# Kernel tuning notes

Measured on AMD Instinct MI355X. Metric: run time of the kernel, lower is better.

Reference implementation:

```python
import jax, jax.numpy as jnp
import numpy as np

D_MODEL = 512
FACTOR = 1
B, L = 32, 2048


def setup_inputs() -> dict:
    key = jax.random.key(0)
    kq, kk, kv = jax.random.split(key, 3)
    query = jax.random.normal(kq, (B, L, D_MODEL), dtype=jnp.float32)
    key_t = jax.random.normal(kk, (B, L, D_MODEL), dtype=jnp.float32)
    value = jax.random.normal(kv, (B, L, D_MODEL), dtype=jnp.float32)
    return {"query": query, "key": key_t, "value": value}


def reference(query, key, value):
    d = D_MODEL
    # FFT-based autocorrelation along the feature (last) axis
    q_fft = jnp.fft.rfft(query, n=d, axis=-1)
    k_fft = jnp.fft.rfft(key, n=d, axis=-1)
    corr = jnp.fft.irfft(q_fft * jnp.conj(k_fft), n=d, axis=-1)  # [B, L, d]

    # top_k = int(factor * log(L)); static because shapes are static
    top_k = int(FACTOR * np.log(value.shape[1]))
    top_vals, _ = jax.lax.top_k(corr, top_k)                      # [B, L, top_k]
    mean_value = jnp.mean(top_vals, axis=-1, keepdims=True)       # [B, L, 1]

    # softmax over the (corr, mean) pair per element
    stacked = jnp.stack(
        [corr, jnp.broadcast_to(mean_value, corr.shape)], axis=-1)  # [B, L, d, 2]
    weights = jax.nn.softmax(stacked, axis=-1)

    # roll values by -1 along the time axis (double-transpose roll in TF source)
    rolled = jnp.roll(value, shift=-1, axis=1)
    out = value * weights[..., 0] + rolled * weights[..., 1]
    return out
```

## Files before the change

kernel.cpp:

```cpp
#include <hip/hip_runtime.h>
#include <math.h>


#define LBITS 11
#define LMASK 2047

typedef float2 cplx;

__device__ __forceinline__ cplx cmul(cplx a, cplx b) {
  return make_float2(a.x * b.x - a.y * b.y, a.x * b.y + a.y * b.x);
}
__device__ __forceinline__ cplx cadd(cplx a, cplx b) {
  return make_float2(a.x + b.x, a.y + b.y);
}
__device__ __forceinline__ cplx csub(cplx a, cplx b) {
  return make_float2(a.x - b.x, a.y - b.y);
}
__device__ __forceinline__ cplx csel(bool c, cplx a, cplx b) {
  return make_float2(c ? a.x : b.x, c ? a.y : b.y);
}
__device__ __forceinline__ cplx cmuli(cplx a, float S) {
  return make_float2(-S * a.y, S * a.x);
}

__device__ __forceinline__ int bitrev6(int x) {
  return (int)(__brev((unsigned)x) >> 26);
}

template<int SIGN>
__device__ __forceinline__ void dft8(cplx* x) {
  const float R = 0.70710678118654752f;
  const float S = (float)SIGN;
  cplx t0 = cadd(x[0], x[4]), t4 = csub(x[0], x[4]);
  cplx t1 = cadd(x[1], x[5]), d1 = csub(x[1], x[5]);
  cplx t2 = cadd(x[2], x[6]), d2 = csub(x[2], x[6]);
  cplx t3 = cadd(x[3], x[7]), d3 = csub(x[3], x[7]);
  cplx t5 = cmul(d1, make_float2(R, S * R));
  cplx t6 = cmuli(d2, S);
  cplx t7 = cmul(d3, make_float2(-R, S * R));
  cplx u0 = cadd(t0, t2), u2 = csub(t0, t2);
  cplx u1 = cadd(t1, t3), u3 = cmuli(csub(t1, t3), S);
  cplx u4 = cadd(t4, t6), u6 = csub(t4, t6);
  cplx u5 = cadd(t5, t7), u7 = cmuli(csub(t5, t7), S);
  cplx v0 = cadd(u0, u1), v1 = csub(u0, u1);
  cplx v2 = cadd(u2, u3), v3 = csub(u2, u3);
  cplx v4 = cadd(u4, u5), v5 = csub(u4, u5);
  cplx v6 = cadd(u6, u7), v7 = csub(u6, u7);
  x[0] = v0; x[1] = v4; x[2] = v2; x[3] = v6;
  x[4] = v1; x[5] = v5; x[6] = v3; x[7] = v7;
}

__device__ __forceinline__ void lane_fft64_dif_fwd(cplx* v, int lane) {
#pragma unroll
  for (int s = 5; s >= 0; --s) {
    const int m = 1 << s;
    const bool hi = (lane & m) != 0;
    float sn, cs;
    __sincosf(-(float)M_PI / (float)m * (float)(lane & (m - 1)), &sn, &cs);
    const cplx w = make_float2(cs, sn);
#pragma unroll
    for (int j = 0; j < 8; ++j) {
      cplx x = v[j], p;
      p.x = __shfl_xor(x.x, m);
      p.y = __shfl_xor(x.y, m);
      cplx sum = cadd(x, p);
      cplx dif = csub(p, x);
      v[j] = csel(hi, cmul(dif, w), sum);
    }
  }
}

__device__ __forceinline__ void lane_fft64_dit_inv(cplx* v, int lane) {
#pragma unroll
  for (int s = 0; s <= 5; ++s) {
    const int m = 1 << s;
    const bool hi = (lane & m) != 0;
    float sn, cs;
    __sincosf((float)M_PI / (float)m * (float)(lane & (m - 1)), &sn, &cs);
    const cplx w = make_float2(cs, sn);
#pragma unroll
    for (int j = 0; j < 8; ++j) {
      cplx x = v[j], p;
      p.x = __shfl_xor(x.x, m);
      p.y = __shfl_xor(x.y, m);
      cplx even = csel(hi, p, x);
      cplx odd  = csel(hi, x, p);
      cplx t = cmul(odd, w);
      v[j] = csel(hi, csub(even, t), cadd(even, t));
    }
  }
}

extern "C" __global__ void __launch_bounds__(256)
autocorr_kernel(const float* __restrict__ q, const float* __restrict__ k,
                const float* __restrict__ vv, float* __restrict__ out) {
  const int lane = (int)threadIdx.x & 63;
  const int wid = (int)threadIdx.x >> 6;
  const int p = (int)blockIdx.x * 4 + wid;
  const int b = p >> LBITS;
  const int l = p & LMASK;
  const size_t base = (size_t)p * 512;

  cplx v[8];
#pragma unroll
  for (int j = 0; j < 8; ++j) {
    const int n = lane + 64 * j;
    v[j] = make_float2(q[base + n], k[base + n]);
  }

  dft8<-1>(v);
  {
    float sn, cs;
    __sincosf(-2.0f * (float)M_PI * (float)lane / 512.0f, &sn, &cs);
    const cplx bw = make_float2(cs, sn);
    cplx w = bw;
#pragma unroll
    for (int j = 1; j < 8; ++j) { v[j] = cmul(v[j], w); w = cmul(w, bw); }
  }
  lane_fft64_dif_fwd(v, lane);

  cplx Bc[8];
#pragma unroll
  for (int k2 = 1; k2 < 8; ++k2) {
    Bc[k2].x = __shfl_xor(v[8 - k2].x, 63);
    Bc[k2].y = __shfl_xor(v[8 - k2].y, 63);
  }
  {
    const int src = bitrev6((64 - bitrev6(lane)) & 63);
    Bc[0].x = __shfl(v[0].x, src);
    Bc[0].y = __shfl(v[0].y, src);
  }

  const float sc = 0.25f / 512.0f;
#pragma unroll
  for (int j = 0; j < 8; ++j) {
    const cplx A = v[j], B = Bc[j];
    const float sr = sc * ((A.x + B.x) * (A.y + B.y) - (A.y - B.y) * (A.x - B.x));
    const float si = sc * ((A.x * A.x - B.x * B.x) + (A.y * A.y - B.y * B.y));
    v[j] = make_float2(sr, si);
  }

  lane_fft64_dit_inv(v, lane);
  {
    float sn, cs;
    __sincosf(2.0f * (float)M_PI * (float)lane / 512.0f, &sn, &cs);
    const cplx bw = make_float2(cs, sn);
    cplx w = bw;
#pragma unroll
    for (int j = 1; j < 8; ++j) { v[j] = cmul(v[j], w); w = cmul(w, bw); }
  }
  dft8<1>(v);

  float vals[8];
#pragma unroll
  for (int j = 0; j < 8; ++j) vals[j] = v[j].x;

  const int pn = (b << LBITS) | ((l + 1) & LMASK);
  const size_t basen = (size_t)pn * 512;
  float va[8], vb[8];
#pragma unroll
  for (int j = 0; j < 8; ++j) {
    const int n = lane + 64 * j;
    va[j] = vv[base + n];
    vb[j] = vv[basen + n];
  }

  float tmp[8];
#pragma unroll
  for (int i = 0; i < 8; ++i) tmp[i] = vals[i];
  float ssum = 0.0f;
  for (int r = 0; r < 7; ++r) {
    float mloc = tmp[0];
#pragma unroll
    for (int i = 1; i < 8; ++i) mloc = fmaxf(mloc, tmp[i]);
    float g = mloc;
#pragma unroll
    for (int off = 32; off >= 1; off >>= 1) g = fmaxf(g, __shfl_xor(g, off));
    ssum += g;
    const unsigned long long ball = __ballot(mloc == g);
    const int firstlane = (int)__ffsll(ball) - 1;
    if (lane == firstlane) {
      bool done = false;
#pragma unroll
      for (int i = 0; i < 8; ++i) {
        if (!done && tmp[i] == g) { tmp[i] = -1e30f; done = true; }
      }
    }
  }
  const float mean = ssum * (1.0f / 7.0f);

#pragma unroll
  for (int j = 0; j < 8; ++j) {
    const float w1 = 1.0f / (1.0f + __expf(vals[j] - mean));
    out[base + lane + 64 * j] = va[j] + (vb[j] - va[j]) * w1;
  }
}

extern "C" void kernel_launch(void* const* d_in, const int* in_sizes, int n_in,
                              void* d_out, int out_size, void* d_ws, size_t ws_size,
                              hipStream_t stream) {
  const float* q = (const float*)d_in[0];
  const float* k = (const float*)d_in[1];
  const float* v = (const float*)d_in[2];
  float* out = (float*)d_out;
  const int positions = 32 * 2048;
  autocorr_kernel<<<dim3(positions / 4), dim3(256), 0, stream>>>(q, k, v, out);
}
```

Before: 444.1 us.

## Use DPP/swizzle cross-lane ops, precomputed twiddles, and threshold-based top-k

```diff
diff --git a/kernel.cpp b/kernel.cpp
--- a/kernel.cpp
+++ b/kernel.cpp
@@ -8,7 +8,7 @@
 typedef float2 cplx;
 
 __device__ __forceinline__ cplx cmul(cplx a, cplx b) {
-  return make_float2(a.x * b.x - a.y * b.y, a.x * b.y + a.y * b.x);
+  return make_float2(fmaf(a.x, b.x, -(a.y * b.y)), fmaf(a.x, b.y, a.y * b.x));
 }
 __device__ __forceinline__ cplx cadd(cplx a, cplx b) {
   return make_float2(a.x + b.x, a.y + b.y);
@@ -16,15 +16,31 @@
 __device__ __forceinline__ cplx csub(cplx a, cplx b) {
   return make_float2(a.x - b.x, a.y - b.y);
 }
-__device__ __forceinline__ cplx csel(bool c, cplx a, cplx b) {
-  return make_float2(c ? a.x : b.x, c ? a.y : b.y);
-}
 __device__ __forceinline__ cplx cmuli(cplx a, float S) {
   return make_float2(-S * a.y, S * a.x);
 }
 
 __device__ __forceinline__ int bitrev6(int x) {
   return (int)(__brev((unsigned)x) >> 26);
+}
+
+template<int M>
+__device__ __forceinline__ float shx(float x, int a32) {
+  const int xi = __float_as_int(x);
+  int r;
+  if constexpr (M == 1)
+    r = __builtin_amdgcn_update_dpp(xi, xi, 0xB1, 0xF, 0xF, false);
+  else if constexpr (M == 2)
+    r = __builtin_amdgcn_update_dpp(xi, xi, 0x4E, 0xF, 0xF, false);
+  else if constexpr (M == 4)
+    r = __builtin_amdgcn_ds_swizzle(xi, 0x101F);
+  else if constexpr (M == 8)
+    r = __builtin_amdgcn_ds_swizzle(xi, 0x201F);
+  else if constexpr (M == 16)
+    r = __builtin_amdgcn_ds_swizzle(xi, 0x401F);
+  else
+    r = __builtin_amdgcn_ds_bpermute(a32, xi);
+  return __int_as_float(r);
 }
 
 template<int SIGN>
@@ -50,45 +66,52 @@
   x[4] = v1; x[5] = v5; x[6] = v3; x[7] = v7;
 }
 
-__device__ __forceinline__ void lane_fft64_dif_fwd(cplx* v, int lane) {
-#pragma unroll
-  for (int s = 5; s >= 0; --s) {
-    const int m = 1 << s;
-    const bool hi = (lane & m) != 0;
-    float sn, cs;
-    __sincosf(-(float)M_PI / (float)m * (float)(lane & (m - 1)), &sn, &cs);
-    const cplx w = make_float2(cs, sn);
-#pragma unroll
-    for (int j = 0; j < 8; ++j) {
-      cplx x = v[j], p;
-      p.x = __shfl_xor(x.x, m);
-      p.y = __shfl_xor(x.y, m);
-      cplx sum = cadd(x, p);
-      cplx dif = csub(p, x);
-      v[j] = csel(hi, cmul(dif, w), sum);
+template<int M>
+__device__ __forceinline__ void fwd_stage(cplx* v, float2 weff, float sgn, int a32) {
+#pragma unroll
+  for (int j = 0; j < 8; ++j) {
+    const float px = shx<M>(v[j].x, a32);
+    const float py = shx<M>(v[j].y, a32);
+    const float prx = fmaf(v[j].x, sgn, px);
+    const float pry = fmaf(v[j].y, sgn, py);
+    if constexpr (M == 1) {
+      v[j] = make_float2(prx, pry);
+    } else {
+      v[j] = make_float2(fmaf(prx, weff.x, -(pry * weff.y)),
+                         fmaf(prx, weff.y, pry * weff.x));
     }
   }
 }
 
-__device__ __forceinline__ void lane_fft64_dit_inv(cplx* v, int lane) {
-#pragma unroll
-  for (int s = 0; s <= 5; ++s) {
-    const int m = 1 << s;
-    const bool hi = (lane & m) != 0;
-    float sn, cs;
-    __sincosf((float)M_PI / (float)m * (float)(lane & (m - 1)), &sn, &cs);
-    const cplx w = make_float2(cs, sn);
-#pragma unroll
-    for (int j = 0; j < 8; ++j) {
-      cplx x = v[j], p;
-      p.x = __shfl_xor(x.x, m);
-      p.y = __shfl_xor(x.y, m);
-      cplx even = csel(hi, p, x);
-      cplx odd  = csel(hi, x, p);
-      cplx t = cmul(odd, w);
-      v[j] = csel(hi, csub(even, t), cadd(even, t));
+template<int M>
+__device__ __forceinline__ void inv_stage(cplx* v, float2 weff, float sgn, int a32) {
+#pragma unroll
+  for (int j = 0; j < 8; ++j) {
+    float ux, uy;
+    if constexpr (M == 1) {
+      ux = v[j].x; uy = v[j].y;
+    } else {
+      ux = fmaf(v[j].x, weff.x, v[j].y * weff.y);
+      uy = fmaf(v[j].y, weff.x, -(v[j].x * weff.y));
     }
-  }
+    const float px = shx<M>(ux, a32);
+    const float py = shx<M>(uy, a32);
+    v[j] = make_float2(fmaf(ux, sgn, px), fmaf(uy, sgn, py));
+  }
+}
+
+__device__ __forceinline__ float wave_max63(float v) {
+#define DPP_MAX(ctrl)                                                        \
+  v = fmaxf(v, __int_as_float(__builtin_amdgcn_update_dpp(                   \
+                   __float_as_int(v), __float_as_int(v), ctrl, 0xF, 0xF, false)));
+  DPP_MAX(0x111)
+  DPP_MAX(0x112)
+  DPP_MAX(0x114)
+  DPP_MAX(0x118)
+  DPP_MAX(0x142)
+  DPP_MAX(0x143)
+#undef DPP_MAX
+  return __int_as_float(__builtin_amdgcn_readlane(__float_as_int(v), 63));
 }
 
 extern "C" __global__ void __launch_bounds__(256)
@@ -101,6 +124,26 @@
   const int l = p & LMASK;
   const size_t base = (size_t)p * 512;
 
+  const int a32 = ((lane ^ 32) << 2);
+  const int a63 = ((lane ^ 63) << 2);
+  const int a0h = (bitrev6((64 - bitrev6(lane)) & 63) << 2);
+
+  float2 w32, w16, w8, w4, w2;
+  {
+    float sn, cs;
+#define MKW(dst, m)                                                          \
+    __sincosf(-(float)M_PI * (float)(lane & ((m)-1)) / (float)(m), &sn, &cs);\
+    dst = (lane & (m)) ? make_float2(cs, sn) : make_float2(1.0f, 0.0f);
+    MKW(w32, 32) MKW(w16, 16) MKW(w8, 8) MKW(w4, 4) MKW(w2, 2)
+#undef MKW
+  }
+  const float s32 = (lane & 32) ? -1.0f : 1.0f;
+  const float s16 = (lane & 16) ? -1.0f : 1.0f;
+  const float s8  = (lane & 8)  ? -1.0f : 1.0f;
+  const float s4  = (lane & 4)  ? -1.0f : 1.0f;
+  const float s2  = (lane & 2)  ? -1.0f : 1.0f;
+  const float s1  = (lane & 1)  ? -1.0f : 1.0f;
+
   cplx v[8];
 #pragma unroll
   for (int j = 0; j < 8; ++j) {
@@ -109,45 +152,54 @@
   }
 
   dft8<-1>(v);
+  float2 bw;
   {
     float sn, cs;
     __sincosf(-2.0f * (float)M_PI * (float)lane / 512.0f, &sn, &cs);
-    const cplx bw = make_float2(cs, sn);
+    bw = make_float2(cs, sn);
     cplx w = bw;
 #pragma unroll
     for (int j = 1; j < 8; ++j) { v[j] = cmul(v[j], w); w = cmul(w, bw); }
   }
-  lane_fft64_dif_fwd(v, lane);
+  fwd_stage<32>(v, w32, s32, a32);
+  fwd_stage<16>(v, w16, s16, a32);
+  fwd_stage<8>(v, w8, s8, a32);
+  fwd_stage<4>(v, w4, s4, a32);
+  fwd_stage<2>(v, w2, s2, a32);
+  fwd_stage<1>(v, w2, s1, a32);
 
   cplx Bc[8];
 #pragma unroll
   for (int k2 = 1; k2 < 8; ++k2) {
-    Bc[k2].x = __shfl_xor(v[8 - k2].x, 63);
-    Bc[k2].y = __shfl_xor(v[8 - k2].y, 63);
-  }
+    Bc[k2].x = __int_as_float(__builtin_amdgcn_ds_bpermute(a63, __float_as_int(v[8 - k2].x)));
+    Bc[k2].y = __int_as_float(__builtin_amdgcn_ds_bpermute(a63, __float_as_int(v[8 - k2].y)));
+  }
+  Bc[0].x = __int_as_float(__builtin_amdgcn_ds_bpermute(a0h, __float_as_int(v[0].x)));
+  Bc[0].y = __int_as_float(__builtin_amdgcn_ds_bpermute(a0h, __float_as_int(v[0].y)));
+
+  const float sc = 0.25f / 512.0f;
+#pragma unroll
+  for (int j = 0; j < 8; ++j) {
+    const cplx A = v[j], B = Bc[j];
+    const float t1 = A.x + B.x, t2 = A.y + B.y, t3 = A.y - B.y, t4 = A.x - B.x;
+    const float sr = sc * fmaf(t1, t2, -(t3 * t4));
+    float si = fmaf(A.x, A.x, -(B.x * B.x));
+    si = fmaf(A.y, A.y, si);
+    si = fmaf(-B.y, B.y, si);
+    v[j] = make_float2(sr, sc * si);
+  }
+
+  inv_stage<1>(v, w2, s1, a32);
+  inv_stage<2>(v, w2, s2, a32);
+  inv_stage<4>(v, w4, s4, a32);
+  inv_stage<8>(v, w8, s8, a32);
+  inv_stage<16>(v, w16, s16, a32);
+  inv_stage<32>(v, w32, s32, a32);
   {
-    const int src = bitrev6((64 - bitrev6(lane)) & 63);
-    Bc[0].x = __shfl(v[0].x, src);
-    Bc[0].y = __shfl(v[0].y, src);
-  }
-
-  const float sc = 0.25f / 512.0f;
-#pragma unroll
-  for (int j = 0; j < 8; ++j) {
-    const cplx A = v[j], B = Bc[j];
-    const float sr = sc * ((A.x + B.x) * (A.y + B.y) - (A.y - B.y) * (A.x - B.x));
-    const float si = sc * ((A.x * A.x - B.x * B.x) + (A.y * A.y - B.y * B.y));
-    v[j] = make_float2(sr, si);
-  }
-
-  lane_fft64_dit_inv(v, lane);
-  {
-    float sn, cs;
-    __sincosf(2.0f * (float)M_PI * (float)lane / 512.0f, &sn, &cs);
-    const cplx bw = make_float2(cs, sn);
-    cplx w = bw;
-#pragma unroll
-    for (int j = 1; j < 8; ++j) { v[j] = cmul(v[j], w); w = cmul(w, bw); }
+    const float2 bwc = make_float2(bw.x, -bw.y);
+    cplx w = bwc;
+#pragma unroll
+    for (int j = 1; j < 8; ++j) { v[j] = cmul(v[j], w); w = cmul(w, bwc); }
   }
   dft8<1>(v);
 
@@ -165,34 +217,30 @@
     vb[j] = vv[basen + n];
   }
 
-  float tmp[8];
-#pragma unroll
-  for (int i = 0; i < 8; ++i) tmp[i] = vals[i];
-  float ssum = 0.0f;
-  for (int r = 0; r < 7; ++r) {
-    float mloc = tmp[0];
-#pragma unroll
-    for (int i = 1; i < 8; ++i) mloc = fmaxf(mloc, tmp[i]);
-    float g = mloc;
-#pragma unroll
-    for (int off = 32; off >= 1; off >>= 1) g = fmaxf(g, __shfl_xor(g, off));
+  float lm = vals[0];
+#pragma unroll
+  for (int i = 1; i < 8; ++i) lm = fmaxf(lm, vals[i]);
+  float g = wave_max63(lm);
+  float ssum = g;
+  float bound = g;
+#pragma unroll
+  for (int r = 1; r < 7; ++r) {
+    lm = -1e30f;
+#pragma unroll
+    for (int i = 0; i < 8; ++i) {
+      const float c = (vals[i] < bound) ? vals[i] : -1e30f;
+      lm = fmaxf(lm, c);
+    }
+    g = wave_max63(lm);
     ssum += g;
-    const unsigned long long ball = __ballot(mloc == g);
-    const int firstlane = (int)__ffsll(ball) - 1;
-    if (lane == firstlane) {
-      bool done = false;
-#pragma unroll
-      for (int i = 0; i < 8; ++i) {
-        if (!done && tmp[i] == g) { tmp[i] = -1e30f; done = true; }
-      }
-    }
+    bound = g;
   }
   const float mean = ssum * (1.0f / 7.0f);
 
 #pragma unroll
   for (int j = 0; j < 8; ++j) {
     const float w1 = 1.0f / (1.0f + __expf(vals[j] - mean));
-    out[base + lane + 64 * j] = va[j] + (vb[j] - va[j]) * w1;
+    out[base + lane + 64 * j] = fmaf(vb[j] - va[j], w1, va[j]);
   }
 }
 
```

After: 401.6 us. -9.6%, faster.
